# Kernel optimization log

Hardware: AMD Instinct MI355X
Metric: run time of the kernel (lower is better)

The kernel has to match this reference:

```python
import jax, jax.numpy as jnp
import numpy as np

# Multi-res hash grid config (tiny-cuda-nn defaults matching input_ch=32 = 16 levels * 2 feats)
L = 16            # n_levels
F = 2             # n_features_per_level
T = 2 ** 19       # hashmap size per level
BASE_RES = 16
FINEST_RES = 512
_b = np.exp((np.log(FINEST_RES) - np.log(BASE_RES)) / (L - 1))
RES = np.floor(BASE_RES * (_b ** np.arange(L))).astype(np.float32)  # (L,)
PRIMES = jnp.array([1, 2654435761, 805459861], dtype=jnp.uint32)
# 8 binary corner offsets of a voxel
CORNERS = jnp.array([[(i >> d) & 1 for d in range(3)] for i in range(8)], dtype=jnp.uint32)  # (8,3)


def hash_encode(x, tables):
    """x: (N,3) in [0,1]; tables: (L, T, F). Returns (N, L*F)."""
    res = jnp.asarray(RES)                              # (L,)
    xs = x[None, :, :] * res[:, None, None]             # (L,N,3) scaled coords
    x0f = jnp.floor(xs)
    frac = xs - x0f                                     # (L,N,3)
    x0 = x0f.astype(jnp.uint32)
    corners = x0[:, :, None, :] + CORNERS[None, None]   # (L,N,8,3) uint32
    # spatial hash: xor of coord*prime, wraparound uint32 mul
    h = (corners[..., 0] * PRIMES[0]) ^ (corners[..., 1] * PRIMES[1]) ^ (corners[..., 2] * PRIMES[2])
    idx = (h % jnp.uint32(T)).astype(jnp.int32)         # (L,N,8)
    gidx = idx + (jnp.arange(L, dtype=jnp.int32) * T)[:, None, None]
    feats = tables.reshape(L * T, F)[gidx]              # (L,N,8,F) gather
    # trilinear weights per corner
    w = jnp.prod(jnp.where(CORNERS[None, None] == 1, frac[:, :, None, :], 1.0 - frac[:, :, None, :]), axis=-1)  # (L,N,8)
    out = jnp.einsum('lnc,lncf->lnf', w, feats)         # (L,N,F)
    return out.transpose(1, 0, 2).reshape(x.shape[0], L * F)


def setup_inputs() -> dict:
    key = jax.random.key(0)
    ks = jax.random.split(key, 16)
    N = 1048576
    W = 128
    pos_flat = jax.random.uniform(ks[0], (N, 3), dtype=jnp.float32)  # world pts in unit cube
    bbox_min = jnp.zeros((3,), dtype=jnp.float32)
    bbox_max = jnp.ones((3,), dtype=jnp.float32)
    tables = jax.random.uniform(ks[1], (L, T, F), dtype=jnp.float32, minval=-1e-4, maxval=1e-4)
    def lin(k, fan_in, fan_out):
        s = 1.0 / np.sqrt(fan_in)
        return jax.random.uniform(k, (fan_in, fan_out), dtype=jnp.float32, minval=-s, maxval=s)
    return {
        'pos_flat': pos_flat, 'bbox_min': bbox_min, 'bbox_max': bbox_max, 'tables': tables,
        'W0': lin(ks[2], L * F, W), 'b0': jnp.zeros((W,), jnp.float32),
        'W1': lin(ks[3], W, W), 'b1': jnp.zeros((W,), jnp.float32),
        'W2': lin(ks[4], W, W), 'b2': jnp.zeros((W,), jnp.float32),
        'W3': lin(ks[5], W, W), 'b3': jnp.zeros((W,), jnp.float32),
        'Wout': lin(ks[6], W, 4), 'bout': jnp.zeros((4,), jnp.float32),
    }


def reference(pos_flat, bbox_min, bbox_max, tables, W0, b0, W1, b1, W2, b2, W3, b3, Wout, bout):
    # normalize into canonical bbox [0,1]^3
    x = (pos_flat - bbox_min) / (bbox_max - bbox_min)
    h = hash_encode(x, tables)                # (N, 32)
    h = jax.nn.relu(h @ W0 + b0)
    h = jax.nn.relu(h @ W1 + b1)
    h = jax.nn.relu(h @ W2 + b2)
    h = jax.nn.relu(h @ W3 + b3)
    raws = h @ Wout + bout                    # (N, 4) rgb + density
    return raws
```

## Files before the change

### kernel.cpp

```cpp
#include <hip/hip_runtime.h>

typedef _Float16 half8 __attribute__((ext_vector_type(8)));
typedef _Float16 half4 __attribute__((ext_vector_type(4)));
typedef _Float16 half2 __attribute__((ext_vector_type(2)));
typedef float    f32x4 __attribute__((ext_vector_type(4)));
typedef float    f32x2 __attribute__((ext_vector_type(2)));
typedef unsigned u32x2 __attribute__((ext_vector_type(2)));
typedef unsigned u32x4 __attribute__((ext_vector_type(4)));

#define TMASK ((1u << 19) - 1u)
#define HSTRIDE 136
constexpr float SCALE = 65536.0f;
constexpr float INV_SCALE = 1.0f / 65536.0f;

__device__ __constant__ unsigned SC_TAB[8]   = {18, 22, 27, 34, 42, 52, 66, 82};
__device__ __constant__ unsigned SX4_TAB[8]  = {5, 6, 7, 9, 11, 13, 17, 21};
__device__ __constant__ unsigned DOFF16_TAB[8] = {0, 1620, 4524, 9627, 20031, 39435, 74587, 148639};
#define DSLOT_TOTAL 289843u

__global__ void prep_dense_kernel(const float* __restrict__ W0, const float* __restrict__ W1,
                                  const float* __restrict__ W2, const float* __restrict__ W3,
                                  const float* __restrict__ Wm,
                                  const float* __restrict__ b0, const float* __restrict__ b1,
                                  const float* __restrict__ b2, const float* __restrict__ b3,
                                  const float* __restrict__ bm,
                                  _Float16* __restrict__ wsW, float* __restrict__ wsB,
                                  const float* __restrict__ tables, _Float16* __restrict__ tabF,
                                  unsigned* __restrict__ dense)
{
    const int bid = (int)blockIdx.x;
    if (bid < 8192) {
        size_t i = (size_t)bid * 256 + threadIdx.x;
        f32x4 v = ((const f32x4*)(tables + (size_t)8 * 524288 * 2))[i];
        half4 o;
        o[0] = (_Float16)(v.x * SCALE);
        o[1] = (_Float16)(v.y * SCALE);
        o[2] = (_Float16)(v.z * SCALE);
        o[3] = (_Float16)(v.w * SCALE);
        ((half4*)tabF)[i] = o;
        return;
    }
    if (bid < 8222) {
        int gid = (bid - 8192) * 256 + threadIdx.x;
        if (gid < 6912) {
            int tile = gid >> 6, lane = gid & 63;
            const float* W; int K, N, toff;
            if (tile < 8)        { W = W0; K = 32;  N = 128; toff = 0;   }
            else if (tile < 40)  { W = W1; K = 128; N = 128; toff = 8;   }
            else if (tile < 72)  { W = W2; K = 128; N = 128; toff = 40;  }
            else if (tile < 104) { W = W3; K = 128; N = 128; toff = 72;  }
            else                 { W = Wm; K = 128; N = 4;   toff = 104; }
            int tt = tile - toff;
            int KT = K >> 5;
            int nt = tt / KT, kt = tt - nt * KT;
            int n = nt * 16 + (lane & 15);
            int kbase = kt * 32 + (lane >> 4) * 8;
            half8 v;
            #pragma unroll
            for (int j = 0; j < 8; j++) {
                int k = kbase + j;
                float w = (n < N) ? W[k * N + n] : 0.0f;
                v[j] = (_Float16)w;
            }
            *(half8*)(wsW + (size_t)gid * 8) = v;
        } else if (gid < 6912 + 528) {
            int i = gid - 6912;
            float v;
            if (i < 512) {
                int layer = i >> 7, n = i & 127;
                const float* b = (layer == 0) ? b0 : (layer == 1) ? b1 : (layer == 2) ? b2 : b3;
                v = b[n] * SCALE;
            } else {
                int n = i - 512;
                v = (n < 4) ? bm[n] * SCALE : 0.0f;
            }
            wsB[i] = v;
        }
        return;
    }
    unsigned e = (unsigned)(bid - 8222) * 256 + threadIdx.x;
    if (e >= DSLOT_TOTAL * 8u) return;
    unsigned brick = e >> 3, j = e & 7u;
    int l = 0;
    #pragma unroll
    for (int i = 1; i < 8; i++) l += (brick >= DOFF16_TAB[i]) ? 1 : 0;
    unsigned local = brick - DOFF16_TAB[l];
    unsigned s = SC_TAB[l], sx4 = SX4_TAB[l];
    unsigned plane = sx4 * s;
    unsigned z = local / plane;
    unsigned rem = local - z * plane;
    unsigned yb = rem / sx4;
    unsigned xs = rem - yb * sx4;
    unsigned x = xs * 4u + (j >> 1);
    unsigned y = yb + (j & 1u);
    unsigned h = (x ^ (y * 2654435761u) ^ (z * 805459861u)) & TMASK;
    const float* src = tables + ((size_t)l * 524288u + h) * 2;
    half2 o; o[0] = (_Float16)(src[0] * SCALE); o[1] = (_Float16)(src[1] * SCALE);
    union { half2 h2; unsigned u; } cv; cv.h2 = o;
    dense[e] = cv.u;
}

__global__ void prep_kernel(const float* __restrict__ W0, const float* __restrict__ W1,
                            const float* __restrict__ W2, const float* __restrict__ W3,
                            const float* __restrict__ Wm,
                            const float* __restrict__ b0, const float* __restrict__ b1,
                            const float* __restrict__ b2, const float* __restrict__ b3,
                            const float* __restrict__ bm,
                            _Float16* __restrict__ wsW, float* __restrict__ wsB,
                            const float* __restrict__ tabSrc, _Float16* __restrict__ tabF,
                            int tabBlocks)
{
    if ((int)blockIdx.x < tabBlocks) {
        size_t i = (size_t)blockIdx.x * 256 + threadIdx.x;
        f32x4 v = ((const f32x4*)tabSrc)[i];
        half4 o;
        o[0] = (_Float16)(v.x * SCALE);
        o[1] = (_Float16)(v.y * SCALE);
        o[2] = (_Float16)(v.z * SCALE);
        o[3] = (_Float16)(v.w * SCALE);
        ((half4*)tabF)[i] = o;
        return;
    }
    int gid = ((int)blockIdx.x - tabBlocks) * 256 + threadIdx.x;
    if (gid < 6912) {
        int tile = gid >> 6, lane = gid & 63;
        const float* W; int K, N, toff;
        if (tile < 8)        { W = W0; K = 32;  N = 128; toff = 0;   }
        else if (tile < 40)  { W = W1; K = 128; N = 128; toff = 8;   }
        else if (tile < 72)  { W = W2; K = 128; N = 128; toff = 40;  }
        else if (tile < 104) { W = W3; K = 128; N = 128; toff = 72;  }
        else                 { W = Wm; K = 128; N = 4;   toff = 104; }
        int tt = tile - toff;
        int KT = K >> 5;
        int nt = tt / KT, kt = tt - nt * KT;
        int n = nt * 16 + (lane & 15);
        int kbase = kt * 32 + (lane >> 4) * 8;
        half8 v;
        #pragma unroll
        for (int j = 0; j < 8; j++) {
            int k = kbase + j;
            float w = (n < N) ? W[k * N + n] : 0.0f;
            v[j] = (_Float16)w;
        }
        *(half8*)(wsW + (size_t)gid * 8) = v;
    } else if (gid < 6912 + 528) {
        int i = gid - 6912;
        float v;
        if (i < 512) {
            int layer = i >> 7, n = i & 127;
            const float* b = (layer == 0) ? b0 : (layer == 1) ? b1 : (layer == 2) ? b2 : b3;
            v = b[n] * SCALE;
        } else {
            int n = i - 512;
            v = (n < 4) ? bm[n] * SCALE : 0.0f;
        }
        wsB[i] = v;
    }
}

struct PtStateB {
    unsigned fI0[4];
    unsigned xm1, fSel;
    unsigned cOff0, cOff1;
    float fF[3], fC[3];
};
struct PtLoadsB {
    u32x4 fB[4]; u32x4 cZ[2]; unsigned fX[4];
};

__global__ __launch_bounds__(256) void encode_brick(
    const float* __restrict__ pos, const float* __restrict__ bmn, const float* __restrict__ bmx,
    const _Float16* __restrict__ tabFine, const unsigned* __restrict__ dense,
    _Float16* __restrict__ feat, int npts)
{
    const int lvl0 = (int)(blockIdx.x & 7);
    const int t = (int)threadIdx.x;
    const long pb = (long)(blockIdx.x >> 3) * 2048 + t;
    const float bx = bmn[0], by = bmn[1], bz = bmn[2];
    const float dxr = bmx[0] - bx, dyr = bmx[1] - by, dzr = bmx[2] - bz;
    constexpr float RESL[16] = {16.f, 20.f, 25.f, 32.f, 40.f, 50.f, 64.f, 80.f,
                                101.f, 128.f, 161.f, 203.f, 256.f, 322.f, 406.f, 512.f};
    const int l1 = lvl0 + 8;
    const _Float16* tblB = tabFine + ((size_t)lvl0 << 20);
    const float resF = RESL[l1], resC = RESL[lvl0];
    const unsigned sx4 = SX4_TAB[lvl0];
    const unsigned plane8 = sx4 * SC_TAB[lvl0] * 8u;
    const unsigned* dlvl = dense + (size_t)DOFF16_TAB[lvl0] * 8u;

    auto computePt = [&](long p, PtStateB& S) {
        const float nx = (pos[p * 3 + 0] - bx) / dxr;
        const float ny = (pos[p * 3 + 1] - by) / dyr;
        const float nz = (pos[p * 3 + 2] - bz) / dzr;
        {
            float xs = nx * resF, ys = ny * resF, zs = nz * resF;
            float fx = floorf(xs), fy = floorf(ys), fz = floorf(zs);
            unsigned xi = (unsigned)fx, yi = (unsigned)fy, zi = (unsigned)fz;
            S.fF[0] = xs - fx; S.fF[1] = ys - fy; S.fF[2] = zs - fz;
            unsigned hy0 = yi * 2654435761u, hy1 = (yi + 1u) * 2654435761u;
            unsigned hz0 = zi * 805459861u,  hz1 = (zi + 1u) * 805459861u;
            unsigned hyz[4] = {hy0 ^ hz0, hy1 ^ hz0, hy0 ^ hz1, hy1 ^ hz1};
            unsigned xm1 = xi ^ (xi + 1u);
            unsigned sel = 0;
            #pragma unroll
            for (int g = 0; g < 4; g++) {
                unsigned i0 = (xi ^ hyz[g]) & TMASK;
                S.fI0[g] = i0;
                sel |= (i0 & 3u) << (2 * g);
            }
            sel |= (xm1 & 3u) << 8;
            if ((xi & 3u) == 3u) sel |= 1024u;
            S.fSel = sel;
            S.xm1 = xm1;
        }
        {
            float xs = nx * resC, ys = ny * resC, zs = nz * resC;
            float fx = floorf(xs), fy = floorf(ys), fz = floorf(zs);
            unsigned xi = (unsigned)fx, yi = (unsigned)fy, zi = (unsigned)fz;
            S.fC[0] = xs - fx; S.fC[1] = ys - fy; S.fC[2] = zs - fz;
            unsigned o0 = ((xi >> 2) + sx4 * yi) * 8u + plane8 * zi + (xi & 3u) * 2u;
            S.cOff0 = o0;
            S.cOff1 = o0 + plane8;
        }
    };

    auto issuePt = [&](const PtStateB& S, PtLoadsB& L) {
        #pragma unroll
        for (int g = 0; g < 4; g++)
            L.fB[g] = *(const u32x4*)(tblB + (size_t)(S.fI0[g] >> 2) * 8);
        __builtin_memcpy(&L.cZ[0], dlvl + S.cOff0, 16);
        __builtin_memcpy(&L.cZ[1], dlvl + S.cOff1, 16);
        if (S.fSel & 1024u) {
            #pragma unroll
            for (int g = 0; g < 4; g++)
                L.fX[g] = *(const unsigned*)(tblB + (size_t)((S.fI0[g] ^ S.xm1) & TMASK) * 2);
        }
    };

    auto consumePt = [&](const PtStateB& S, const PtLoadsB& L, long p) {
        {
            float tx = S.fF[0], ty = S.fF[1], tz = S.fF[2];
            float wyz[4] = {(1.0f - ty) * (1.0f - tz), ty * (1.0f - tz),
                            (1.0f - ty) * tz,          ty * tz};
            unsigned selw = S.fSel;
            unsigned m = (selw >> 8) & 3u;
            bool carry = (selw & 1024u) != 0u;
            float b0 = 0.0f, b1 = 0.0f;
            #pragma unroll
            for (int g = 0; g < 4; g++) {
                u32x4 v = L.fB[g];
                unsigned s0 = (selw >> (2 * g)) & 3u;
                unsigned s1 = s0 ^ m;
                unsigned a0_ = (s0 & 2u) ? v[2] : v[0];
                unsigned b0_ = (s0 & 2u) ? v[3] : v[1];
                unsigned e0  = (s0 & 1u) ? b0_ : a0_;
                unsigned a1_ = (s1 & 2u) ? v[2] : v[0];
                unsigned b1_ = (s1 & 2u) ? v[3] : v[1];
                unsigned e1s = (s1 & 1u) ? b1_ : a1_;
                unsigned e1  = carry ? L.fX[g] : e1s;
                union { unsigned u; half2 h; } u0, u1;
                u0.u = e0; u1.u = e1;
                float w0 = wyz[g] * (1.0f - tx), w1 = wyz[g] * tx;
                b0 += w0 * (float)u0.h[0] + w1 * (float)u1.h[0];
                b1 += w0 * (float)u0.h[1] + w1 * (float)u1.h[1];
            }
            half2 ov2; ov2[0] = (_Float16)b0; ov2[1] = (_Float16)b1;
            union { half2 h; unsigned u; } cv; cv.h = ov2;
            __builtin_nontemporal_store(cv.u, (unsigned*)(feat + ((size_t)l1 * npts + p) * 2));
        }
        {
            float tx = S.fC[0], ty = S.fC[1], tz = S.fC[2];
            float wyz[4] = {(1.0f - ty) * (1.0f - tz), ty * (1.0f - tz),
                            (1.0f - ty) * tz,          ty * tz};
            float a0 = 0.0f, a1 = 0.0f;
            #pragma unroll
            for (int g = 0; g < 4; g++) {
                union { unsigned u; half2 h; } u0, u1;
                u0.u = L.cZ[g >> 1][g & 1];
                u1.u = L.cZ[g >> 1][2 + (g & 1)];
                float w0 = wyz[g] * (1.0f - tx), w1 = wyz[g] * tx;
                a0 += w0 * (float)u0.h[0] + w1 * (float)u1.h[0];
                a1 += w0 * (float)u0.h[1] + w1 * (float)u1.h[1];
            }
            half2 ov2; ov2[0] = (_Float16)a0; ov2[1] = (_Float16)a1;
            union { half2 h; unsigned u; } cv; cv.h = ov2;
            __builtin_nontemporal_store(cv.u, (unsigned*)(feat + ((size_t)lvl0 * npts + p) * 2));
        }
    };

    PtStateB sA, sB; PtLoadsB lA, lB;
    computePt(pb + 0 * 256, sA); issuePt(sA, lA);
    computePt(pb + 1 * 256, sB); issuePt(sB, lB);
    #pragma unroll
    for (int k = 0; k < 6; k++) {
        if ((k & 1) == 0) {
            consumePt(sA, lA, pb + (long)k * 256);
            computePt(pb + (long)(k + 2) * 256, sA); issuePt(sA, lA);
        } else {
            consumePt(sB, lB, pb + (long)k * 256);
            computePt(pb + (long)(k + 2) * 256, sB); issuePt(sB, lB);
        }
    }
    consumePt(sA, lA, pb + 6 * 256);
    consumePt(sB, lB, pb + 7 * 256);
}

#define ELANE 68

template<int KT, int TOFF>
__device__ __forceinline__ void layer_fwd4(half8 b[4][4], const half8* __restrict__ wf,
                                           const float* __restrict__ wsB, int li,
                                           unsigned* __restrict__ eb, int lane, int quad,
                                           unsigned srcA, unsigned srcB, int mtbase)
{
    unsigned* wptr = eb + lane * ELANE;
    #pragma unroll
    for (int mt = 0; mt < 8; mt++) {
        f32x4 bias = *(const f32x4*)&wsB[li * 128 + mt * 16 + quad * 4];
        half8 w[KT];
        #pragma unroll
        for (int kt = 0; kt < KT; kt++)
            w[kt] = wf[(size_t)(TOFF + mt * KT + kt) * 64 + lane];
        f32x4 acc[4] = {bias, bias, bias, bias};
        #pragma unroll
        for (int nt = 0; nt < 4; nt++)
            #pragma unroll
            for (int kt = 0; kt < KT; kt++)
                acc[nt] = __builtin_amdgcn_mfma_f32_16x16x32_f16(w[kt], b[nt][kt], acc[nt], 0, 0, 0);
        #pragma unroll
        for (int np = 0; np < 2; np++) {
            union { _Float16 h[8]; u32x4 v; } pk;
            #pragma unroll
            for (int r = 0; r < 4; r++) {
                pk.h[r]     = (_Float16)fmaxf(acc[2 * np][r],     0.0f);
                pk.h[4 + r] = (_Float16)fmaxf(acc[2 * np + 1][r], 0.0f);
            }
            *(u32x4*)(wptr + mt * 8 + np * 4) = pk.v;
        }
    }
    #pragma unroll
    for (int ktp = 0; ktp < 4; ktp++) {
        int mt = 2 * ktp + mtbase;
        u32x4 rA0 = *(const u32x4*)(eb + srcA * ELANE + mt * 8);
        u32x4 rA1 = *(const u32x4*)(eb + srcA * ELANE + mt * 8 + 4);
        u32x4 rB0 = *(const u32x4*)(eb + srcB * ELANE + mt * 8);
        u32x4 rB1 = *(const u32x4*)(eb + srcB * ELANE + mt * 8 + 4);
        union { u32x4 v; half8 h; } c0, c1, c2, c3;
        c0.v = (u32x4){rA0[0], rA0[1], rB0[0], rB0[1]};
        c1.v = (u32x4){rA0[2], rA0[3], rB0[2], rB0[3]};
        c2.v = (u32x4){rA1[0], rA1[1], rB1[0], rB1[1]};
        c3.v = (u32x4){rA1[2], rA1[3], rB1[2], rB1[3]};
        b[0][ktp] = c0.h;
        b[1][ktp] = c1.h;
        b[2][ktp] = c2.h;
        b[3][ktp] = c3.h;
    }
}

__global__ __launch_bounds__(256, 2) void mlp_kernel(
    const unsigned* __restrict__ feat32, const half8* __restrict__ wf,
    const float* __restrict__ wsB, float* __restrict__ out, int npts)
{
    __shared__ __align__(16) unsigned ebuf[4 * 64 * ELANE];
    const int t = threadIdx.x;
    const int lane = t & 63, wv = t >> 6;
    const int col = lane & 15, quad = lane >> 4;
    const long base = (long)blockIdx.x * 256 + wv * 64;
    unsigned* eb = ebuf + wv * (64 * ELANE);
    const int q1 = 2 * (quad & 1);
    const unsigned srcA = (unsigned)(col + 16 * q1);
    const unsigned srcB = (unsigned)(col + 16 * (q1 + 1));
    const int mtbase = quad >> 1;

    half8 b[4][4];
    #pragma unroll
    for (int nt = 0; nt < 4; nt++) {
        const long pt = base + nt * 16 + col;
        union { unsigned u4[4]; half8 v; } cv;
        #pragma unroll
        for (int jj = 0; jj < 4; jj++)
            cv.u4[jj] = feat32[(size_t)(quad * 4 + jj) * npts + pt];
        b[nt][0] = cv.v;
    }

    layer_fwd4<1, 0 >(b, wf, wsB, 0, eb, lane, quad, srcA, srcB, mtbase);
    layer_fwd4<4, 8 >(b, wf, wsB, 1, eb, lane, quad, srcA, srcB, mtbase);
    layer_fwd4<4, 40>(b, wf, wsB, 2, eb, lane, quad, srcA, srcB, mtbase);
    layer_fwd4<4, 72>(b, wf, wsB, 3, eb, lane, quad, srcA, srcB, mtbase);

    f32x4 biaso = *(const f32x4*)&wsB[512 + quad * 4];
    f32x4 acco[4] = {biaso, biaso, biaso, biaso};
    #pragma unroll
    for (int kt = 0; kt < 4; kt++) {
        half8 w = wf[(size_t)(104 + kt) * 64 + lane];
        #pragma unroll
        for (int nt = 0; nt < 4; nt++)
            acco[nt] = __builtin_amdgcn_mfma_f32_16x16x32_f16(w, b[nt][kt], acco[nt], 0, 0, 0);
    }
    if (quad == 0) {
        #pragma unroll
        for (int nt = 0; nt < 4; nt++) {
            f32x4 v;
            #pragma unroll
            for (int r = 0; r < 4; r++) v[r] = acco[nt][r] * INV_SCALE;
            *(f32x4*)(out + (base + nt * 16 + col) * 4) = v;
        }
    }
}

template<int KT, int TOFF, bool RELU>
__device__ __forceinline__ void mlp_layer(_Float16* h, const half8* __restrict__ wf,
                                          const float* __restrict__ wsB, int layerIdx,
                                          int m0, int lane)
{
    const int col = lane & 15, quad = lane >> 4;
    const int sw = (col & 3) << 3;
    half8 a[2][KT];
    #pragma unroll
    for (int mt = 0; mt < 2; mt++)
        #pragma unroll
        for (int kt = 0; kt < KT; kt++)
            a[mt][kt] = *(const half8*)&h[(m0 + mt * 16 + col) * HSTRIDE + ((kt * 32 + quad * 8) ^ sw)];
    f32x4 acc[2][8];
    #pragma unroll
    for (int nt = 0; nt < 8; nt++) {
        float bv = wsB[layerIdx * 128 + nt * 16 + col];
        acc[0][nt] = (f32x4){bv, bv, bv, bv};
        acc[1][nt] = (f32x4){bv, bv, bv, bv};
    }
    #pragma unroll
    for (int nt = 0; nt < 8; nt++) {
        half8 b[KT];
        #pragma unroll
        for (int kt = 0; kt < KT; kt++)
            b[kt] = wf[(size_t)(TOFF + nt * KT + kt) * 64 + lane];
        #pragma unroll
        for (int mt = 0; mt < 2; mt++)
            #pragma unroll
            for (int kt = 0; kt < KT; kt++)
                acc[mt][nt] = __builtin_amdgcn_mfma_f32_16x16x32_f16(a[mt][kt], b[kt], acc[mt][nt], 0, 0, 0);
    }
    #pragma unroll
    for (int mt = 0; mt < 2; mt++)
        #pragma unroll
        for (int nt = 0; nt < 8; nt++) {
            f32x4 v = acc[mt][nt];
            #pragma unroll
            for (int r = 0; r < 4; r++) {
                float x = v[r];
                if (RELU) x = fmaxf(x, 0.0f);
                h[(m0 + mt * 16 + quad * 4 + r) * HSTRIDE + ((nt * 16 + col) ^ (r << 3))] = (_Float16)x;
            }
        }
}

__global__ __launch_bounds__(256, 2) void fused_kernel(
    const float* __restrict__ pos, const float* __restrict__ bmn, const float* __restrict__ bmx,
    const float* __restrict__ tables, const half8* __restrict__ wf, const float* __restrict__ wsB,
    float* __restrict__ out)
{
    __shared__ _Float16 hbuf[128 * HSTRIDE];
    __shared__ float outstage[512];
    const int t = threadIdx.x;
    const long base = (long)blockIdx.x * 128;
    {
        const int p = t >> 1, hh = t & 1;
        const long gp = base + p;
        const float b0x = bmn[0], b0y = bmn[1], b0z = bmn[2];
        const float nx = (pos[gp * 3 + 0] - b0x) / (bmx[0] - b0x);
        const float ny = (pos[gp * 3 + 1] - b0y) / (bmx[1] - b0y);
        const float nz = (pos[gp * 3 + 2] - b0z) / (bmx[2] - b0z);
        constexpr float RLO[8] = {16.f, 20.f, 25.f, 32.f, 40.f, 50.f, 64.f, 80.f};
        constexpr float RHI[8] = {101.f, 128.f, 161.f, 203.f, 256.f, 322.f, 406.f, 512.f};
        half8 fa, fb;
        #pragma unroll
        for (int li = 0; li < 8; li++) {
            const float res = hh ? RHI[li] : RLO[li];
            const float* tbl = tables + ((size_t)(hh * 8 + li) << 20);
            float xs = nx * res, ys = ny * res, zs = nz * res;
            float fx = floorf(xs), fy = floorf(ys), fz = floorf(zs);
            unsigned xi = (unsigned)fx, yi = (unsigned)fy, zi = (unsigned)fz;
            float tx = xs - fx, ty = ys - fy, tz = zs - fz;
            unsigned hx[2] = {xi, xi + 1u};
            unsigned hy[2] = {yi * 2654435761u, (yi + 1u) * 2654435761u};
            unsigned hz[2] = {zi * 805459861u, (zi + 1u) * 805459861u};
            float wx[2] = {1.0f - tx, tx}, wy[2] = {1.0f - ty, ty}, wz[2] = {1.0f - tz, tz};
            float a0 = 0.0f, a1 = 0.0f;
            #pragma unroll
            for (int c = 0; c < 8; c++) {
                unsigned hsh = hx[c & 1] ^ hy[(c >> 1) & 1] ^ hz[c >> 2];
                unsigned idx = hsh & TMASK;
                f32x2 f = *(const f32x2*)(tbl + (size_t)idx * 2);
                float w = wx[c & 1] * wy[(c >> 1) & 1] * wz[c >> 2];
                a0 += w * f.x;
                a1 += w * f.y;
            }
            if (li < 4) { fa[2 * li]       = (_Float16)(a0 * SCALE); fa[2 * li + 1]       = (_Float16)(a1 * SCALE); }
            else        { fb[2 * (li - 4)] = (_Float16)(a0 * SCALE); fb[2 * (li - 4) + 1] = (_Float16)(a1 * SCALE); }
        }
        const int sw = (p & 3) << 3;
        *(half8*)&hbuf[p * HSTRIDE + ((hh * 16) ^ sw)]       = fa;
        *(half8*)&hbuf[p * HSTRIDE + (((hh * 16) + 8) ^ sw)] = fb;
    }
    __syncthreads();
    {
        const int lane = t & 63;
        const int m0 = (t >> 6) * 32;
        mlp_layer<1, 0,   true>(hbuf, wf, wsB, 0, m0, lane);
        mlp_layer<4, 8,   true>(hbuf, wf, wsB, 1, m0, lane);
        mlp_layer<4, 40,  true>(hbuf, wf, wsB, 2, m0, lane);
        mlp_layer<4, 72,  true>(hbuf, wf, wsB, 3, m0, lane);
        const int col = lane & 15, quad = lane >> 4;
        const int sw = (col & 3) << 3;
        half8 a[2][4];
        #pragma unroll
        for (int mt = 0; mt < 2; mt++)
            #pragma unroll
            for (int kt = 0; kt < 4; kt++)
                a[mt][kt] = *(const half8*)&hbuf[(m0 + mt * 16 + col) * HSTRIDE + ((kt * 32 + quad * 8) ^ sw)];
        float bv = wsB[512 + col];
        f32x4 acc[2] = {(f32x4){bv, bv, bv, bv}, (f32x4){bv, bv, bv, bv}};
        #pragma unroll
        for (int kt = 0; kt < 4; kt++) {
            half8 bfr = wf[(size_t)(104 + kt) * 64 + lane];
            #pragma unroll
            for (int mt = 0; mt < 2; mt++)
                acc[mt] = __builtin_amdgcn_mfma_f32_16x16x32_f16(a[mt][kt], bfr, acc[mt], 0, 0, 0);
        }
        if (col < 4) {
            #pragma unroll
            for (int mt = 0; mt < 2; mt++)
                #pragma unroll
                for (int r = 0; r < 4; r++)
                    outstage[(m0 + mt * 16 + quad * 4 + r) * 4 + col] = acc[mt][r] * INV_SCALE;
        }
    }
    __syncthreads();
    if (t < 128) {
        f32x4 v = ((const f32x4*)outstage)[t];
        *(f32x4*)(out + (base + t) * 4) = v;
    }
}

extern "C" void kernel_launch(void* const* d_in, const int* in_sizes, int n_in,
                              void* d_out, int out_size, void* d_ws, size_t ws_size,
                              hipStream_t stream) {
    const float* pos    = (const float*)d_in[0];
    const float* bmn    = (const float*)d_in[1];
    const float* bmx    = (const float*)d_in[2];
    const float* tables = (const float*)d_in[3];
    const float* W0 = (const float*)d_in[4];
    const float* b0 = (const float*)d_in[5];
    const float* W1 = (const float*)d_in[6];
    const float* b1 = (const float*)d_in[7];
    const float* W2 = (const float*)d_in[8];
    const float* b2 = (const float*)d_in[9];
    const float* W3 = (const float*)d_in[10];
    const float* b3 = (const float*)d_in[11];
    const float* Wm = (const float*)d_in[12];
    const float* bm = (const float*)d_in[13];

    const int N = in_sizes[0] / 3;
    const size_t featBytes    = (size_t)N * 16 * 4;
    const size_t tabFineBytes = (size_t)8 * 524288 * 2 * 2;
    const size_t denseBytesB  = ((size_t)DSLOT_TOTAL * 32 + 255) & ~(size_t)255;
    const size_t needB = featBytes + tabFineBytes + denseBytesB + 110592 + 2112;

    if (ws_size >= needB && (N % 2048) == 0) {
        _Float16* feat  = (_Float16*)d_ws;
        _Float16* tabF  = (_Float16*)((char*)d_ws + featBytes);
        unsigned* dense = (unsigned*)((char*)d_ws + featBytes + tabFineBytes);
        _Float16* wsW   = (_Float16*)((char*)d_ws + featBytes + tabFineBytes + denseBytesB);
        float*    wsB   = (float*)((char*)d_ws + featBytes + tabFineBytes + denseBytesB + 110592);
        prep_dense_kernel<<<8192 + 30 + (DSLOT_TOTAL * 8 + 255) / 256, 256, 0, stream>>>(
            W0, W1, W2, W3, Wm, b0, b1, b2, b3, bm, wsW, wsB, tables, tabF, dense);
        encode_brick<<<(N / 2048) * 8, 256, 0, stream>>>(pos, bmn, bmx, tabF,
                                                         dense, feat, N);
        mlp_kernel<<<N / 256, 256, 0, stream>>>((const unsigned*)feat, (const half8*)wsW,
                                                wsB, (float*)d_out, N);
    } else {
        _Float16* wsW = (_Float16*)d_ws;
        float*    wsB = (float*)((char*)d_ws + 110592);
        prep_kernel<<<30, 256, 0, stream>>>(W0, W1, W2, W3, Wm, b0, b1, b2, b3, bm,
                                            wsW, wsB, tables, (_Float16*)nullptr, 0);
        fused_kernel<<<N / 128, 256, 0, stream>>>(pos, bmn, bmx, tables,
                                                  (const half8*)wsW, wsB, (float*)d_out);
    }
}
```

Measured before the change: 508.1 us.

## Stage MLP weights through shared memory with register prefetch per layer

Instead of each wave reading every layer's fp16 weight fragments straight from global memory, the block cooperatively copies each layer's weights into a shared buffer. The next layer's weights are prefetched into registers while the current layer computes. The change adds barriers between layers, 32KB of extra LDS and register pressure from the staging array. It also drops the min-blocks-per-CU hint from the launch bounds, which may lower occupancy.

Measured after the change: 566.7 us. 11.5% more time.

```diff
diff --git a/kernel.cpp b/kernel.cpp
--- a/kernel.cpp
+++ b/kernel.cpp
@@ -306,8 +306,8 @@
 
 #define ELANE 68
 
-template<int KT, int TOFF>
-__device__ __forceinline__ void layer_fwd4(half8 b[4][4], const half8* __restrict__ wf,
+template<int KT>
+__device__ __forceinline__ void layer_fwd4(half8 b[4][4], const half8* wl,
                                            const float* __restrict__ wsB, int li,
                                            unsigned* __restrict__ eb, int lane, int quad,
                                            unsigned srcA, unsigned srcB, int mtbase)
@@ -319,7 +319,7 @@
         half8 w[KT];
         #pragma unroll
         for (int kt = 0; kt < KT; kt++)
-            w[kt] = wf[(size_t)(TOFF + mt * KT + kt) * 64 + lane];
+            w[kt] = wl[(mt * KT + kt) * 64 + lane];
         f32x4 acc[4] = {bias, bias, bias, bias};
         #pragma unroll
         for (int nt = 0; nt < 4; nt++)
@@ -356,11 +356,13 @@
     }
 }
 
-__global__ __launch_bounds__(256, 2) void mlp_kernel(
+__global__ __launch_bounds__(256) void mlp_kernel(
     const unsigned* __restrict__ feat32, const half8* __restrict__ wf,
     const float* __restrict__ wsB, float* __restrict__ out, int npts)
 {
     __shared__ __align__(16) unsigned ebuf[4 * 64 * ELANE];
+    __shared__ __align__(16) _Float16 wbuf_raw[2048 * 8];
+    half8* wbuf = (half8*)wbuf_raw;
     const int t = threadIdx.x;
     const int lane = t & 63, wv = t >> 6;
     const int col = lane & 15, quad = lane >> 4;
@@ -371,6 +373,13 @@
     const unsigned srcB = (unsigned)(col + 16 * (q1 + 1));
     const int mtbase = quad >> 1;
 
+    {
+        half8 s0 = wf[t];
+        half8 s1 = wf[256 + t];
+        wbuf[t] = s0;
+        wbuf[256 + t] = s1;
+    }
+
     half8 b[4][4];
     #pragma unroll
     for (int nt = 0; nt < 4; nt++) {
@@ -381,17 +390,45 @@
             cv.u4[jj] = feat32[(size_t)(quad * 4 + jj) * npts + pt];
         b[nt][0] = cv.v;
     }
-
-    layer_fwd4<1, 0 >(b, wf, wsB, 0, eb, lane, quad, srcA, srcB, mtbase);
-    layer_fwd4<4, 8 >(b, wf, wsB, 1, eb, lane, quad, srcA, srcB, mtbase);
-    layer_fwd4<4, 40>(b, wf, wsB, 2, eb, lane, quad, srcA, srcB, mtbase);
-    layer_fwd4<4, 72>(b, wf, wsB, 3, eb, lane, quad, srcA, srcB, mtbase);
+    __syncthreads();
+
+    half8 stg[8];
+
+    #pragma unroll
+    for (int i = 0; i < 8; i++) stg[i] = wf[512 + i * 256 + t];
+    layer_fwd4<1>(b, wbuf, wsB, 0, eb, lane, quad, srcA, srcB, mtbase);
+    __syncthreads();
+    #pragma unroll
+    for (int i = 0; i < 8; i++) wbuf[i * 256 + t] = stg[i];
+    __syncthreads();
+
+    #pragma unroll
+    for (int i = 0; i < 8; i++) stg[i] = wf[2560 + i * 256 + t];
+    layer_fwd4<4>(b, wbuf, wsB, 1, eb, lane, quad, srcA, srcB, mtbase);
+    __syncthreads();
+    #pragma unroll
+    for (int i = 0; i < 8; i++) wbuf[i * 256 + t] = stg[i];
+    __syncthreads();
+
+    #pragma unroll
+    for (int i = 0; i < 8; i++) stg[i] = wf[4608 + i * 256 + t];
+    layer_fwd4<4>(b, wbuf, wsB, 2, eb, lane, quad, srcA, srcB, mtbase);
+    __syncthreads();
+    #pragma unroll
+    for (int i = 0; i < 8; i++) wbuf[i * 256 + t] = stg[i];
+    __syncthreads();
+
+    half8 so = wf[6656 + t];
+    layer_fwd4<4>(b, wbuf, wsB, 3, eb, lane, quad, srcA, srcB, mtbase);
+    __syncthreads();
+    wbuf[t] = so;
+    __syncthreads();
 
     f32x4 biaso = *(const f32x4*)&wsB[512 + quad * 4];
     f32x4 acco[4] = {biaso, biaso, biaso, biaso};
     #pragma unroll
     for (int kt = 0; kt < 4; kt++) {
-        half8 w = wf[(size_t)(104 + kt) * 64 + lane];
+        half8 w = wbuf[kt * 64 + lane];
         #pragma unroll
         for (int nt = 0; nt < 4; nt++)
             acco[nt] = __builtin_amdgcn_mfma_f32_16x16x32_f16(w, b[nt][kt], acco[nt], 0, 0, 0);
```
